# Performance work log

Hardware: AMD Instinct MI355X
Metric: run time of the kernel (lower is better)

The kernel has to match this reference:

```python
import jax, jax.numpy as jnp
import numpy as np

B, T, D, H, C = 128, 1024, 256, 256, 128


def setup_inputs() -> dict:
    key = jax.random.key(0)
    ks = jax.random.split(key, 10)
    s = 0.02  # scale down randn init so sigmoid/tanh don't saturate numerically
    inp = {
        "x": jax.random.normal(ks[0], (B, T, D), dtype=jnp.float32),
        "W_xi": jax.random.normal(ks[1], (D, H), dtype=jnp.float32) * s,
        "W_hi": jax.random.normal(ks[2], (H, H), dtype=jnp.float32) * s,
        "b_i": jnp.zeros((H,), jnp.float32),
        "W_xf": jax.random.normal(ks[3], (D, H), dtype=jnp.float32) * s,
        "W_hf": jax.random.normal(ks[4], (H, H), dtype=jnp.float32) * s,
        "b_f": jnp.zeros((H,), jnp.float32),
        "W_xg": jax.random.normal(ks[5], (D, H), dtype=jnp.float32) * s,
        "W_hg": jax.random.normal(ks[6], (H, H), dtype=jnp.float32) * s,
        "b_g": jnp.zeros((H,), jnp.float32),
        "W_xo": jax.random.normal(ks[7], (D, H), dtype=jnp.float32) * s,
        "W_ho": jax.random.normal(ks[8], (H, H), dtype=jnp.float32) * s,
        "b_o": jnp.zeros((H,), jnp.float32),
        "W_hy": jax.random.normal(ks[9], (H, C), dtype=jnp.float32) * s,
        "b_y": jnp.zeros((C,), jnp.float32),
    }
    return inp


def reference(x, W_xi, W_hi, b_i, W_xf, W_hf, b_f, W_xg, W_hg, b_g,
              W_xo, W_ho, b_o, W_hy, b_y):
    batch, _, _ = x.shape
    hid = W_hi.shape[0]
    # Precompute all input projections for all timesteps (4 big GEMMs).
    xi = jnp.einsum("btd,dh->bth", x, W_xi) + b_i
    xf = jnp.einsum("btd,dh->bth", x, W_xf) + b_f
    xg = jnp.einsum("btd,dh->bth", x, W_xg) + b_g
    xo = jnp.einsum("btd,dh->bth", x, W_xo) + b_o
    # Time-major stacked gate pre-activations: [T, B, 4H]
    gates_x = jnp.concatenate([xi, xf, xg, xo], axis=-1).transpose(1, 0, 2)
    W_h = jnp.concatenate([W_hi, W_hf, W_hg, W_ho], axis=1)  # [H, 4H]

    def step(carry, gx_t):
        h, c = carry
        z = gx_t + h @ W_h  # [B, 4H]
        i_t = jax.nn.sigmoid(z[:, 0 * hid:1 * hid])
        f_t = jax.nn.sigmoid(z[:, 1 * hid:2 * hid])
        g_t = jnp.tanh(z[:, 2 * hid:3 * hid])
        o_t = jax.nn.sigmoid(z[:, 3 * hid:4 * hid])
        c_new = f_t * c + i_t * g_t
        h_new = o_t * jnp.tanh(c_new)
        return (h_new, c_new), None

    h0 = jnp.zeros((batch, hid), x.dtype)
    c0 = jnp.zeros((batch, hid), x.dtype)
    (h_T, _), _ = jax.lax.scan(step, (h0, c0), gates_x)
    return h_T @ W_hy + b_y
```

## Files before the change

kernel.cpp:

```cpp
#include <hip/hip_runtime.h>

using u16 = unsigned short;
using u32 = unsigned int;

typedef _Float16 f16x2 __attribute__((ext_vector_type(2)));
typedef _Float16 f16x8 __attribute__((ext_vector_type(8)));
typedef float    f32x4 __attribute__((ext_vector_type(4)));

__device__ __forceinline__ u16 f16bits(float x) {
  union { _Float16 h; u16 u; } r; r.h = (_Float16)x; return r.u;
}
__device__ __forceinline__ float h2f(u16 v) {
  union { u16 u; _Float16 h; } r; r.u = v; return (float)r.h;
}
__device__ __forceinline__ u32 pack2(float a, float b) {
  union { f16x2 h; u32 u; } r; r.h.x = (_Float16)a; r.h.y = (_Float16)b; return r.u;
}
__device__ __forceinline__ float fdot2a(u32 a, u32 b, float c) {
  union { u32 u; f16x2 h; } ua, ub; ua.u = a; ub.u = b;
#if __has_builtin(__builtin_amdgcn_fdot2)
  return __builtin_amdgcn_fdot2(ua.h, ub.h, c, false);
#else
  return c + (float)ua.h.x * (float)ub.h.x + (float)ua.h.y * (float)ub.h.y;
#endif
}
__device__ __forceinline__ float sigmoidf_(float x) { return 1.0f / (1.0f + __expf(-x)); }
__device__ __forceinline__ float tanhf_(float x)    { return 1.0f - 2.0f / (__expf(2.0f * x) + 1.0f); }

__device__ __forceinline__ f16x8 lds16(const u16* p) {
  union { uint4 u; f16x8 h; } r; r.u = *(const uint4*)p; return r.h;
}

__global__ void lstm_prep(const float* __restrict__ Wxi, const float* __restrict__ Wxf,
                          const float* __restrict__ Wxg, const float* __restrict__ Wxo,
                          const float* __restrict__ Whi, const float* __restrict__ Whf,
                          const float* __restrict__ Whg, const float* __restrict__ Who,
                          u16* __restrict__ WxT, u32* __restrict__ Whpp,
                          u32* __restrict__ h16s, float* __restrict__ c_s) {
  int idx = blockIdx.x * 256 + threadIdx.x;
  if (idx < 262144) {
    int n = idx >> 8, k = idx & 255;
    int g = n >> 8;
    const float* W = (g == 0) ? Wxi : (g == 1) ? Wxf : (g == 2) ? Wxg : Wxo;
    WxT[idx] = f16bits(W[k * 256 + (n & 255)]);
  } else if (idx < 262144 + 131072) {
    int i2 = idx - 262144;
    int e = i2 & 3, tmp = i2 >> 2;
    int t = tmp & 1023, i4 = tmp >> 10;
    int cc = i4 >> 3, pp = i4 & 7;
    int w = t >> 6, l = t & 63, q = l >> 4;
    int j = w * 64 + (l & 15) * 4 + cc;
    int kk = q * 32 + pp * 4 + e;
    int g = j >> 8, col = j & 255;
    const float* W = (g == 0) ? Whi : (g == 1) ? Whf : (g == 2) ? Whg : Who;
    u32 lo = f16bits(W[(2 * kk) * 256 + col]);
    u32 hi = f16bits(W[(2 * kk + 1) * 256 + col]);
    Whpp[i2] = lo | (hi << 16);
  } else if (idx < 262144 + 131072 + 16384) {
    h16s[idx - 393216] = 0u;
  } else if (idx < 262144 + 131072 + 16384 + 32768) {
    c_s[idx - 409600] = 0.0f;
  }
}

__global__ __launch_bounds__(256) void proj_gemm(
    const float* __restrict__ x, const u16* __restrict__ WxT,
    u16* __restrict__ gates, const float* __restrict__ bi,
    const float* __restrict__ bf, const float* __restrict__ bg,
    const float* __restrict__ bo, int t0, int tcShift) {
  __shared__ u16 Al[128 * 72];
  __shared__ u16 Bl[128 * 72];
  const int tid = threadIdx.x;
  const int lane = tid & 63, wv = tid >> 6;
  const int wr = wv >> 1, wc = wv & 1;
  const int m0 = blockIdx.x * 128, n0 = blockIdx.y * 128;
  const int tcMask = (1 << tcShift) - 1;
  f32x4 acc[4][4] = {};
  for (int k0 = 0; k0 < 256; k0 += 64) {
#pragma unroll
    for (int p = 0; p < 8; ++p) {
      int flat = p * 256 + tid;
      int r = flat >> 4, cc = flat & 15;
      int m = m0 + r;
      int b = m >> tcShift, tc = m & tcMask;
      const float4 xv = *(const float4*)(x + (size_t)(b * 1024 + t0 + tc) * 256 + k0 + cc * 4);
      uint2 w2 = make_uint2(pack2(xv.x, xv.y), pack2(xv.z, xv.w));
      *(uint2*)&Al[r * 72 + cc * 4] = w2;
    }
#pragma unroll
    for (int p = 0; p < 8; ++p) {
      int flat = p * 256 + tid;
      int r = flat >> 4, cc = flat & 15;
      uint2 w2 = *(const uint2*)(WxT + (size_t)(n0 + r) * 256 + k0 + cc * 4);
      *(uint2*)&Bl[r * 72 + cc * 4] = w2;
    }
    __syncthreads();
#pragma unroll
    for (int kk = 0; kk < 64; kk += 32) {
      f16x8 af[4], bfr[4];
#pragma unroll
      for (int i = 0; i < 4; ++i) {
        af[i]  = lds16(&Al[(wr * 64 + i * 16 + (lane & 15)) * 72 + kk + (lane >> 4) * 8]);
        bfr[i] = lds16(&Bl[(wc * 64 + i * 16 + (lane & 15)) * 72 + kk + (lane >> 4) * 8]);
      }
#pragma unroll
      for (int mi = 0; mi < 4; ++mi)
#pragma unroll
        for (int ni = 0; ni < 4; ++ni)
          acc[mi][ni] = __builtin_amdgcn_mfma_f32_16x16x32_f16(af[mi], bfr[ni], acc[mi][ni], 0, 0, 0);
    }
    __syncthreads();
  }
#pragma unroll
  for (int ni = 0; ni < 4; ++ni) {
    int n = n0 + wc * 64 + ni * 16 + (lane & 15);
    int g = n >> 8;
    const float* bp = (g == 0) ? bi : (g == 1) ? bf : (g == 2) ? bg : bo;
    float bias = bp[n & 255];
#pragma unroll
    for (int mi = 0; mi < 4; ++mi) {
#pragma unroll
      for (int ri = 0; ri < 4; ++ri) {
        int m = m0 + wr * 64 + mi * 16 + (lane >> 4) * 4 + ri;
        gates[(size_t)m * 1024 + n] = f16bits(acc[mi][ni][ri] + bias);
      }
    }
  }
}

__global__ __launch_bounds__(1024) void lstm_rec(
    const u32* __restrict__ Whpp, const u16* __restrict__ gates,
    u32* __restrict__ h16s, float* __restrict__ c_s,
    const float* __restrict__ Why, const float* __restrict__ by,
    float* __restrict__ out, int Tc, int last) {
  extern __shared__ unsigned char smem[];
  uint4* ldsW = (uint4*)smem;
  u32*   hq   = (u32*)(smem + 131072);
  float* zbuf = (float*)(smem + 131072 + 1152);
  const int b = blockIdx.x, t = threadIdx.x;
  const int l = t & 63, w = t >> 6, q = l >> 4;
  const int jb = w * 64 + (l & 15) * 4;

  u32 wreg[96];
  const uint4* Wp4 = (const uint4*)Whpp;
#pragma unroll
  for (int i4 = 0; i4 < 32; ++i4) {
    uint4 v = Wp4[i4 * 1024 + t];
    const int cc = i4 >> 3, pp = i4 & 7;
    if (pp < 6) {
      wreg[cc * 24 + pp * 4 + 0] = v.x;
      wreg[cc * 24 + pp * 4 + 1] = v.y;
      wreg[cc * 24 + pp * 4 + 2] = v.z;
      wreg[cc * 24 + pp * 4 + 3] = v.w;
    } else {
      ldsW[(cc * 2 + pp - 6) * 1024 + t] = v;
    }
  }
  if (t < 128) hq[(t >> 5) * 36 + (t & 31)] = h16s[b * 128 + t];
  float c = 0.0f;
  if (t < 256) c = c_s[b * 256 + t];
  const u16* gxp = gates + (size_t)b * Tc * 1024 + jb;
  int buf = 0;
  __syncthreads();

  for (int tc = 0; tc < Tc; ++tc) {
    uint2 gx = *(const uint2*)(gxp + (size_t)tc * 1024);
    float acc0 = 0.f, acc1 = 0.f, acc2 = 0.f, acc3 = 0.f;
    const uint4* hb = (const uint4*)(hq + buf * 144 + q * 36);
#pragma unroll
    for (int u = 0; u < 8; ++u) {
      uint4 hv = hb[u];
      uint4 w0, w1, w2, w3;
      if (u < 6) {
        w0 = make_uint4(wreg[0 * 24 + u * 4], wreg[0 * 24 + u * 4 + 1], wreg[0 * 24 + u * 4 + 2], wreg[0 * 24 + u * 4 + 3]);
        w1 = make_uint4(wreg[1 * 24 + u * 4], wreg[1 * 24 + u * 4 + 1], wreg[1 * 24 + u * 4 + 2], wreg[1 * 24 + u * 4 + 3]);
        w2 = make_uint4(wreg[2 * 24 + u * 4], wreg[2 * 24 + u * 4 + 1], wreg[2 * 24 + u * 4 + 2], wreg[2 * 24 + u * 4 + 3]);
        w3 = make_uint4(wreg[3 * 24 + u * 4], wreg[3 * 24 + u * 4 + 1], wreg[3 * 24 + u * 4 + 2], wreg[3 * 24 + u * 4 + 3]);
      } else {
        w0 = ldsW[(0 * 2 + u - 6) * 1024 + t];
        w1 = ldsW[(1 * 2 + u - 6) * 1024 + t];
        w2 = ldsW[(2 * 2 + u - 6) * 1024 + t];
        w3 = ldsW[(3 * 2 + u - 6) * 1024 + t];
      }
      acc0 = fdot2a(hv.x, w0.x, acc0); acc0 = fdot2a(hv.y, w0.y, acc0);
      acc0 = fdot2a(hv.z, w0.z, acc0); acc0 = fdot2a(hv.w, w0.w, acc0);
      acc1 = fdot2a(hv.x, w1.x, acc1); acc1 = fdot2a(hv.y, w1.y, acc1);
      acc1 = fdot2a(hv.z, w1.z, acc1); acc1 = fdot2a(hv.w, w1.w, acc1);
      acc2 = fdot2a(hv.x, w2.x, acc2); acc2 = fdot2a(hv.y, w2.y, acc2);
      acc2 = fdot2a(hv.z, w2.z, acc2); acc2 = fdot2a(hv.w, w2.w, acc2);
      acc3 = fdot2a(hv.x, w3.x, acc3); acc3 = fdot2a(hv.y, w3.y, acc3);
      acc3 = fdot2a(hv.z, w3.z, acc3); acc3 = fdot2a(hv.w, w3.w, acc3);
    }
    acc0 += __shfl_xor(acc0, 16); acc0 += __shfl_xor(acc0, 32);
    acc1 += __shfl_xor(acc1, 16); acc1 += __shfl_xor(acc1, 32);
    acc2 += __shfl_xor(acc2, 16); acc2 += __shfl_xor(acc2, 32);
    acc3 += __shfl_xor(acc3, 16); acc3 += __shfl_xor(acc3, 32);
    if (l < 16) {
      float4 z4;
      z4.x = acc0 + h2f((u16)(gx.x & 0xffff));
      z4.y = acc1 + h2f((u16)(gx.x >> 16));
      z4.z = acc2 + h2f((u16)(gx.y & 0xffff));
      z4.w = acc3 + h2f((u16)(gx.y >> 16));
      *(float4*)&zbuf[jb] = z4;
    }
    __syncthreads();
    if (t < 256) {
      float zi = zbuf[t], zf = zbuf[t + 256], zg = zbuf[t + 512], zo = zbuf[t + 768];
      float i_ = sigmoidf_(zi), f_ = sigmoidf_(zf), g_ = tanhf_(zg), o_ = sigmoidf_(zo);
      c = f_ * c + i_ * g_;
      float h_ = o_ * tanhf_(c);
      const int kk = t >> 1, qq = kk >> 5, pp = kk & 31;
      ((u16*)(hq + (buf ^ 1) * 144))[(qq * 36 + pp) * 2 + (t & 1)] = f16bits(h_);
    }
    buf ^= 1;
    __syncthreads();
  }

  if (t < 128) h16s[b * 128 + t] = hq[buf * 144 + (t >> 5) * 36 + (t & 31)];
  if (t < 256) c_s[b * 256 + t] = c;

  if (last && t < 128) {
    float acc = by[t];
    const u16* hh = (const u16*)(hq + buf * 144);
#pragma unroll 8
    for (int k = 0; k < 256; ++k) {
      float hv = h2f(hh[((k >> 6) * 36 + ((k >> 1) & 31)) * 2 + (k & 1)]);
      acc += hv * Why[k * 128 + t];
    }
    out[b * 128 + t] = acc;
  }
}

extern "C" void kernel_launch(void* const* d_in, const int* in_sizes, int n_in,
                              void* d_out, int out_size, void* d_ws, size_t ws_size,
                              hipStream_t stream) {
  const float* x   = (const float*)d_in[0];
  const float* Wxi = (const float*)d_in[1];
  const float* Whi = (const float*)d_in[2];
  const float* b_i = (const float*)d_in[3];
  const float* Wxf = (const float*)d_in[4];
  const float* Whf = (const float*)d_in[5];
  const float* b_f = (const float*)d_in[6];
  const float* Wxg = (const float*)d_in[7];
  const float* Whg = (const float*)d_in[8];
  const float* b_g = (const float*)d_in[9];
  const float* Wxo = (const float*)d_in[10];
  const float* Who = (const float*)d_in[11];
  const float* b_o = (const float*)d_in[12];
  const float* Why = (const float*)d_in[13];
  const float* b_y = (const float*)d_in[14];
  float* out = (float*)d_out;

  int Tc = 256;
  while (Tc > 32 && (size_t)128 * Tc * 1024 * 2 + 1245184ull > ws_size) Tc >>= 1;
  const int tcShift = __builtin_ctz((unsigned)Tc);
  const int nch = 1024 / Tc;

  char* wsb = (char*)d_ws;
  const size_t gbytes = (size_t)128 * Tc * 1024 * 2;
  u16*   gates16 = (u16*)wsb;
  u16*   WxT     = (u16*)(wsb + gbytes);
  u32*   Whpp    = (u32*)(wsb + gbytes + 524288);
  u32*   h16s    = (u32*)(wsb + gbytes + 1048576);
  float* c_s     = (float*)(wsb + gbytes + 1048576 + 65536);

  const int recLds = 131072 + 1152 + 4096;
  (void)hipFuncSetAttribute((const void*)lstm_rec,
                            hipFuncAttributeMaxDynamicSharedMemorySize, recLds);

  lstm_prep<<<1728, 256, 0, stream>>>(Wxi, Wxf, Wxg, Wxo, Whi, Whf, Whg, Who,
                                      WxT, Whpp, h16s, c_s);
  for (int ci = 0; ci < nch; ++ci) {
    int t0 = ci * Tc;
    proj_gemm<<<dim3(Tc, 8), 256, 0, stream>>>(x, WxT, gates16, b_i, b_f, b_g, b_o,
                                               t0, tcShift);
    lstm_rec<<<128, 1024, recLds, stream>>>(Whpp, gates16, h16s, c_s, Why, b_y, out,
                                            Tc, (ci == nch - 1) ? 1 : 0);
  }
}
```

Before: 2.254 ms.

## Assign one hidden unit's four gates per lane to drop mid-step barrier

The recurrent weight packing is remapped so each 16-lane column group computes the i/f/g/o pre-activations for a single hidden unit instead of four adjacent gate columns. Each thread can then apply the nonlinearities and cell update in registers right after the shuffle reduction, which removes the zbuf round-trip through LDS and one __syncthreads per timestep. It also keeps 7 of 8 weight chunks in registers (112 VGPRs) instead of 6, halving LDS weight traffic, and prefetches the next step's gate inputs one iteration ahead. The costs are higher register pressure and redundant activation math in all four q-lanes, with only the l<16 lanes writing h.

```diff
diff --git a/kernel.cpp b/kernel.cpp
--- a/kernel.cpp
+++ b/kernel.cpp
@@ -47,11 +47,10 @@
     int i2 = idx - 262144;
     int e = i2 & 3, tmp = i2 >> 2;
     int t = tmp & 1023, i4 = tmp >> 10;
-    int cc = i4 >> 3, pp = i4 & 7;
+    int g = i4 >> 3, pp = i4 & 7;
     int w = t >> 6, l = t & 63, q = l >> 4;
-    int j = w * 64 + (l & 15) * 4 + cc;
+    int col = w * 16 + (l & 15);
     int kk = q * 32 + pp * 4 + e;
-    int g = j >> 8, col = j & 255;
     const float* W = (g == 0) ? Whi : (g == 1) ? Whf : (g == 2) ? Whg : Who;
     u32 lo = f16bits(W[(2 * kk) * 256 + col]);
     u32 hi = f16bits(W[(2 * kk + 1) * 256 + col]);
@@ -135,52 +134,55 @@
     float* __restrict__ out, int Tc, int last) {
   extern __shared__ unsigned char smem[];
   uint4* ldsW = (uint4*)smem;
-  u32*   hq   = (u32*)(smem + 131072);
-  float* zbuf = (float*)(smem + 131072 + 1152);
+  u32*   hq   = (u32*)(smem + 65536);
   const int b = blockIdx.x, t = threadIdx.x;
   const int l = t & 63, w = t >> 6, q = l >> 4;
-  const int jb = w * 64 + (l & 15) * 4;
-
-  u32 wreg[96];
+  const int hcol = w * 16 + (l & 15);
+
+  u32 wreg[112];
   const uint4* Wp4 = (const uint4*)Whpp;
 #pragma unroll
   for (int i4 = 0; i4 < 32; ++i4) {
     uint4 v = Wp4[i4 * 1024 + t];
-    const int cc = i4 >> 3, pp = i4 & 7;
-    if (pp < 6) {
-      wreg[cc * 24 + pp * 4 + 0] = v.x;
-      wreg[cc * 24 + pp * 4 + 1] = v.y;
-      wreg[cc * 24 + pp * 4 + 2] = v.z;
-      wreg[cc * 24 + pp * 4 + 3] = v.w;
+    const int g = i4 >> 3, pp = i4 & 7;
+    if (pp < 7) {
+      wreg[g * 28 + pp * 4 + 0] = v.x;
+      wreg[g * 28 + pp * 4 + 1] = v.y;
+      wreg[g * 28 + pp * 4 + 2] = v.z;
+      wreg[g * 28 + pp * 4 + 3] = v.w;
     } else {
-      ldsW[(cc * 2 + pp - 6) * 1024 + t] = v;
-    }
-  }
-  if (t < 128) hq[(t >> 5) * 36 + (t & 31)] = h16s[b * 128 + t];
-  float c = 0.0f;
-  if (t < 256) c = c_s[b * 256 + t];
-  const u16* gxp = gates + (size_t)b * Tc * 1024 + jb;
+      ldsW[g * 1024 + t] = v;
+    }
+  }
+  if (t < 128) hq[(t >> 5) * 40 + (t & 31)] = h16s[b * 128 + t];
+  float c = c_s[b * 256 + hcol];
+  const u16* gxp = gates + (size_t)b * Tc * 1024 + hcol;
+  u16 pre0 = gxp[0], pre1 = gxp[256], pre2 = gxp[512], pre3 = gxp[768];
   int buf = 0;
   __syncthreads();
 
   for (int tc = 0; tc < Tc; ++tc) {
-    uint2 gx = *(const uint2*)(gxp + (size_t)tc * 1024);
+    const u16 cur0 = pre0, cur1 = pre1, cur2 = pre2, cur3 = pre3;
+    if (tc + 1 < Tc) {
+      const u16* gn = gxp + (size_t)(tc + 1) * 1024;
+      pre0 = gn[0]; pre1 = gn[256]; pre2 = gn[512]; pre3 = gn[768];
+    }
     float acc0 = 0.f, acc1 = 0.f, acc2 = 0.f, acc3 = 0.f;
-    const uint4* hb = (const uint4*)(hq + buf * 144 + q * 36);
+    const uint4* hb = (const uint4*)(hq + buf * 160 + q * 40);
 #pragma unroll
     for (int u = 0; u < 8; ++u) {
       uint4 hv = hb[u];
       uint4 w0, w1, w2, w3;
-      if (u < 6) {
-        w0 = make_uint4(wreg[0 * 24 + u * 4], wreg[0 * 24 + u * 4 + 1], wreg[0 * 24 + u * 4 + 2], wreg[0 * 24 + u * 4 + 3]);
-        w1 = make_uint4(wreg[1 * 24 + u * 4], wreg[1 * 24 + u * 4 + 1], wreg[1 * 24 + u * 4 + 2], wreg[1 * 24 + u * 4 + 3]);
-        w2 = make_uint4(wreg[2 * 24 + u * 4], wreg[2 * 24 + u * 4 + 1], wreg[2 * 24 + u * 4 + 2], wreg[2 * 24 + u * 4 + 3]);
-        w3 = make_uint4(wreg[3 * 24 + u * 4], wreg[3 * 24 + u * 4 + 1], wreg[3 * 24 + u * 4 + 2], wreg[3 * 24 + u * 4 + 3]);
+      if (u < 7) {
+        w0 = make_uint4(wreg[0 * 28 + u * 4], wreg[0 * 28 + u * 4 + 1], wreg[0 * 28 + u * 4 + 2], wreg[0 * 28 + u * 4 + 3]);
+        w1 = make_uint4(wreg[1 * 28 + u * 4], wreg[1 * 28 + u * 4 + 1], wreg[1 * 28 + u * 4 + 2], wreg[1 * 28 + u * 4 + 3]);
+        w2 = make_uint4(wreg[2 * 28 + u * 4], wreg[2 * 28 + u * 4 + 1], wreg[2 * 28 + u * 4 + 2], wreg[2 * 28 + u * 4 + 3]);
+        w3 = make_uint4(wreg[3 * 28 + u * 4], wreg[3 * 28 + u * 4 + 1], wreg[3 * 28 + u * 4 + 2], wreg[3 * 28 + u * 4 + 3]);
       } else {
-        w0 = ldsW[(0 * 2 + u - 6) * 1024 + t];
-        w1 = ldsW[(1 * 2 + u - 6) * 1024 + t];
-        w2 = ldsW[(2 * 2 + u - 6) * 1024 + t];
-        w3 = ldsW[(3 * 2 + u - 6) * 1024 + t];
+        w0 = ldsW[0 * 1024 + t];
+        w1 = ldsW[1 * 1024 + t];
+        w2 = ldsW[2 * 1024 + t];
+        w3 = ldsW[3 * 1024 + t];
       }
       acc0 = fdot2a(hv.x, w0.x, acc0); acc0 = fdot2a(hv.y, w0.y, acc0);
       acc0 = fdot2a(hv.z, w0.z, acc0); acc0 = fdot2a(hv.w, w0.w, acc0);
@@ -195,36 +197,30 @@
     acc1 += __shfl_xor(acc1, 16); acc1 += __shfl_xor(acc1, 32);
     acc2 += __shfl_xor(acc2, 16); acc2 += __shfl_xor(acc2, 32);
     acc3 += __shfl_xor(acc3, 16); acc3 += __shfl_xor(acc3, 32);
+    float zi = acc0 + h2f(cur0);
+    float zf = acc1 + h2f(cur1);
+    float zg = acc2 + h2f(cur2);
+    float zo = acc3 + h2f(cur3);
+    float i_ = sigmoidf_(zi), f_ = sigmoidf_(zf), g_ = tanhf_(zg), o_ = sigmoidf_(zo);
+    c = f_ * c + i_ * g_;
+    float h_ = o_ * tanhf_(c);
     if (l < 16) {
-      float4 z4;
-      z4.x = acc0 + h2f((u16)(gx.x & 0xffff));
-      z4.y = acc1 + h2f((u16)(gx.x >> 16));
-      z4.z = acc2 + h2f((u16)(gx.y & 0xffff));
-      z4.w = acc3 + h2f((u16)(gx.y >> 16));
-      *(float4*)&zbuf[jb] = z4;
-    }
-    __syncthreads();
-    if (t < 256) {
-      float zi = zbuf[t], zf = zbuf[t + 256], zg = zbuf[t + 512], zo = zbuf[t + 768];
-      float i_ = sigmoidf_(zi), f_ = sigmoidf_(zf), g_ = tanhf_(zg), o_ = sigmoidf_(zo);
-      c = f_ * c + i_ * g_;
-      float h_ = o_ * tanhf_(c);
-      const int kk = t >> 1, qq = kk >> 5, pp = kk & 31;
-      ((u16*)(hq + (buf ^ 1) * 144))[(qq * 36 + pp) * 2 + (t & 1)] = f16bits(h_);
+      const int kk = hcol >> 1;
+      ((u16*)hq)[((buf ^ 1) * 160 + (kk >> 5) * 40 + (kk & 31)) * 2 + (hcol & 1)] = f16bits(h_);
     }
     buf ^= 1;
     __syncthreads();
   }
 
-  if (t < 128) h16s[b * 128 + t] = hq[buf * 144 + (t >> 5) * 36 + (t & 31)];
-  if (t < 256) c_s[b * 256 + t] = c;
+  if (t < 128) h16s[b * 128 + t] = hq[buf * 160 + (t >> 5) * 40 + (t & 31)];
+  if (l < 16) c_s[b * 256 + hcol] = c;
 
   if (last && t < 128) {
     float acc = by[t];
-    const u16* hh = (const u16*)(hq + buf * 144);
+    const u16* hh = (const u16*)(hq + buf * 160);
 #pragma unroll 8
     for (int k = 0; k < 256; ++k) {
-      float hv = h2f(hh[((k >> 6) * 36 + ((k >> 1) & 31)) * 2 + (k & 1)]);
+      float hv = h2f(hh[((k >> 6) * 40 + ((k >> 1) & 31)) * 2 + (k & 1)]);
       acc += hv * Why[k * 128 + t];
     }
     out[b * 128 + t] = acc;
@@ -264,7 +260,7 @@
   u32*   h16s    = (u32*)(wsb + gbytes + 1048576);
   float* c_s     = (float*)(wsb + gbytes + 1048576 + 65536);
 
-  const int recLds = 131072 + 1152 + 4096;
+  const int recLds = 65536 + 1280;
   (void)hipFuncSetAttribute((const void*)lstm_rec,
                             hipFuncAttributeMaxDynamicSharedMemorySize, recLds);
 
```

Result: slower. 4.365 ms (+93.7%).

## Repartition LSTM recurrence so each wave owns a K-quarter and reduces via LDS

Applied to the files above, without the earlier changes.

Changes the recurrent matvec partition so each 4-wave group covers 256 gate columns. Each wave handles one quarter of the hidden dimension, and h values are broadcast with readlane instead of per-lane LDS vector reads. Cross-lane shuffle reductions are replaced by per-wave partial sums written to LDS and summed by the 256 cell threads. Gate pre-activations are now written interleaved (i,f,g,o per column) and prefetched one step ahead. The change also adds s_setprio around the dot-product loop. In exchange it uses more LDS and adds a four-way LDS reduction in the serial section.

```diff
diff --git a/kernel.cpp b/kernel.cpp
--- a/kernel.cpp
+++ b/kernel.cpp
@@ -48,9 +48,10 @@
     int e = i2 & 3, tmp = i2 >> 2;
     int t = tmp & 1023, i4 = tmp >> 10;
     int cc = i4 >> 3, pp = i4 & 7;
-    int w = t >> 6, l = t & 63, q = l >> 4;
-    int j = w * 64 + (l & 15) * 4 + cc;
-    int kk = q * 32 + pp * 4 + e;
+    int w = t >> 6, l = t & 63;
+    int grp = w >> 2, qw = w & 3;
+    int j = grp * 256 + l * 4 + cc;
+    int kk = qw * 32 + pp * 4 + e;
     int g = j >> 8, col = j & 255;
     const float* W = (g == 0) ? Whi : (g == 1) ? Whf : (g == 2) ? Whg : Who;
     u32 lo = f16bits(W[(2 * kk) * 256 + col]);
@@ -117,12 +118,13 @@
     int g = n >> 8;
     const float* bp = (g == 0) ? bi : (g == 1) ? bf : (g == 2) ? bg : bo;
     float bias = bp[n & 255];
+    const int nperm = (n & 255) * 4 + g;
 #pragma unroll
     for (int mi = 0; mi < 4; ++mi) {
 #pragma unroll
       for (int ri = 0; ri < 4; ++ri) {
         int m = m0 + wr * 64 + mi * 16 + (lane >> 4) * 4 + ri;
-        gates[(size_t)m * 1024 + n] = f16bits(acc[mi][ni][ri] + bias);
+        gates[(size_t)m * 1024 + nperm] = f16bits(acc[mi][ni][ri] + bias);
       }
     }
   }
@@ -134,12 +136,13 @@
     const float* __restrict__ Why, const float* __restrict__ by,
     float* __restrict__ out, int Tc, int last) {
   extern __shared__ unsigned char smem[];
-  uint4* ldsW = (uint4*)smem;
-  u32*   hq   = (u32*)(smem + 131072);
-  float* zbuf = (float*)(smem + 131072 + 1152);
+  uint4* ldsW  = (uint4*)smem;
+  u32*   hq    = (u32*)(smem + 131072);
+  float* zpart = (float*)(smem + 131072 + 1280);
   const int b = blockIdx.x, t = threadIdx.x;
-  const int l = t & 63, w = t >> 6, q = l >> 4;
-  const int jb = w * 64 + (l & 15) * 4;
+  const int l = t & 63, w = t >> 6;
+  const int grp = w >> 2, qw = w & 3;
+  const int jb = grp * 256 + l * 4;
 
   u32 wreg[96];
   const uint4* Wp4 = (const uint4*)Whpp;
@@ -153,78 +156,90 @@
       wreg[cc * 24 + pp * 4 + 2] = v.z;
       wreg[cc * 24 + pp * 4 + 3] = v.w;
     } else {
-      ldsW[(cc * 2 + pp - 6) * 1024 + t] = v;
-    }
-  }
-  if (t < 128) hq[(t >> 5) * 36 + (t & 31)] = h16s[b * 128 + t];
+      ldsW[(cc * 2 + (pp - 6)) * 1024 + t] = v;
+    }
+  }
+  if (t < 128) hq[(t >> 5) * 40 + (t & 31)] = h16s[b * 128 + t];
   float c = 0.0f;
-  if (t < 256) c = c_s[b * 256 + t];
-  const u16* gxp = gates + (size_t)b * Tc * 1024 + jb;
+  uint2 pre = make_uint2(0u, 0u);
+  const u16* gxp = gates + (size_t)b * Tc * 1024 + t * 4;
+  if (t < 256) {
+    c = c_s[b * 256 + t];
+    pre = *(const uint2*)gxp;
+  }
   int buf = 0;
   __syncthreads();
 
   for (int tc = 0; tc < Tc; ++tc) {
-    uint2 gx = *(const uint2*)(gxp + (size_t)tc * 1024);
-    float acc0 = 0.f, acc1 = 0.f, acc2 = 0.f, acc3 = 0.f;
-    const uint4* hb = (const uint4*)(hq + buf * 144 + q * 36);
-#pragma unroll
-    for (int u = 0; u < 8; ++u) {
-      uint4 hv = hb[u];
-      uint4 w0, w1, w2, w3;
-      if (u < 6) {
-        w0 = make_uint4(wreg[0 * 24 + u * 4], wreg[0 * 24 + u * 4 + 1], wreg[0 * 24 + u * 4 + 2], wreg[0 * 24 + u * 4 + 3]);
-        w1 = make_uint4(wreg[1 * 24 + u * 4], wreg[1 * 24 + u * 4 + 1], wreg[1 * 24 + u * 4 + 2], wreg[1 * 24 + u * 4 + 3]);
-        w2 = make_uint4(wreg[2 * 24 + u * 4], wreg[2 * 24 + u * 4 + 1], wreg[2 * 24 + u * 4 + 2], wreg[2 * 24 + u * 4 + 3]);
-        w3 = make_uint4(wreg[3 * 24 + u * 4], wreg[3 * 24 + u * 4 + 1], wreg[3 * 24 + u * 4 + 2], wreg[3 * 24 + u * 4 + 3]);
-      } else {
-        w0 = ldsW[(0 * 2 + u - 6) * 1024 + t];
-        w1 = ldsW[(1 * 2 + u - 6) * 1024 + t];
-        w2 = ldsW[(2 * 2 + u - 6) * 1024 + t];
-        w3 = ldsW[(3 * 2 + u - 6) * 1024 + t];
-      }
-      acc0 = fdot2a(hv.x, w0.x, acc0); acc0 = fdot2a(hv.y, w0.y, acc0);
-      acc0 = fdot2a(hv.z, w0.z, acc0); acc0 = fdot2a(hv.w, w0.w, acc0);
-      acc1 = fdot2a(hv.x, w1.x, acc1); acc1 = fdot2a(hv.y, w1.y, acc1);
-      acc1 = fdot2a(hv.z, w1.z, acc1); acc1 = fdot2a(hv.w, w1.w, acc1);
-      acc2 = fdot2a(hv.x, w2.x, acc2); acc2 = fdot2a(hv.y, w2.y, acc2);
-      acc2 = fdot2a(hv.z, w2.z, acc2); acc2 = fdot2a(hv.w, w2.w, acc2);
-      acc3 = fdot2a(hv.x, w3.x, acc3); acc3 = fdot2a(hv.y, w3.y, acc3);
-      acc3 = fdot2a(hv.z, w3.z, acc3); acc3 = fdot2a(hv.w, w3.w, acc3);
-    }
-    acc0 += __shfl_xor(acc0, 16); acc0 += __shfl_xor(acc0, 32);
-    acc1 += __shfl_xor(acc1, 16); acc1 += __shfl_xor(acc1, 32);
-    acc2 += __shfl_xor(acc2, 16); acc2 += __shfl_xor(acc2, 32);
-    acc3 += __shfl_xor(acc3, 16); acc3 += __shfl_xor(acc3, 32);
-    if (l < 16) {
-      float4 z4;
-      z4.x = acc0 + h2f((u16)(gx.x & 0xffff));
-      z4.y = acc1 + h2f((u16)(gx.x >> 16));
-      z4.z = acc2 + h2f((u16)(gx.y & 0xffff));
-      z4.w = acc3 + h2f((u16)(gx.y >> 16));
-      *(float4*)&zbuf[jb] = z4;
-    }
+    const uint4 hv4 = *(const uint4*)(hq + buf * 160 + qw * 40 + (l & 7) * 4);
+    u32 sh[32];
+#pragma unroll
+    for (int i = 0; i < 8; ++i) {
+      sh[4 * i + 0] = (u32)__builtin_amdgcn_readlane((int)hv4.x, i);
+      sh[4 * i + 1] = (u32)__builtin_amdgcn_readlane((int)hv4.y, i);
+      sh[4 * i + 2] = (u32)__builtin_amdgcn_readlane((int)hv4.z, i);
+      sh[4 * i + 3] = (u32)__builtin_amdgcn_readlane((int)hv4.w, i);
+    }
+    float acc[4] = {0.f, 0.f, 0.f, 0.f};
+    __builtin_amdgcn_s_setprio(1);
+#pragma unroll
+    for (int pp = 0; pp < 6; ++pp) {
+#pragma unroll
+      for (int cc = 0; cc < 4; ++cc) {
+        acc[cc] = fdot2a(sh[pp * 4 + 0], wreg[cc * 24 + pp * 4 + 0], acc[cc]);
+        acc[cc] = fdot2a(sh[pp * 4 + 1], wreg[cc * 24 + pp * 4 + 1], acc[cc]);
+        acc[cc] = fdot2a(sh[pp * 4 + 2], wreg[cc * 24 + pp * 4 + 2], acc[cc]);
+        acc[cc] = fdot2a(sh[pp * 4 + 3], wreg[cc * 24 + pp * 4 + 3], acc[cc]);
+      }
+    }
+#pragma unroll
+    for (int pp = 6; pp < 8; ++pp) {
+#pragma unroll
+      for (int cc = 0; cc < 4; ++cc) {
+        uint4 wv = ldsW[(cc * 2 + (pp - 6)) * 1024 + t];
+        acc[cc] = fdot2a(sh[pp * 4 + 0], wv.x, acc[cc]);
+        acc[cc] = fdot2a(sh[pp * 4 + 1], wv.y, acc[cc]);
+        acc[cc] = fdot2a(sh[pp * 4 + 2], wv.z, acc[cc]);
+        acc[cc] = fdot2a(sh[pp * 4 + 3], wv.w, acc[cc]);
+      }
+    }
+    __builtin_amdgcn_s_setprio(0);
+    *(float4*)&zpart[qw * 1024 + jb] = *(float4*)acc;
     __syncthreads();
     if (t < 256) {
-      float zi = zbuf[t], zf = zbuf[t + 256], zg = zbuf[t + 512], zo = zbuf[t + 768];
+      const uint2 gx = pre;
+      if (tc + 1 < Tc) pre = *(const uint2*)(gxp + (size_t)(tc + 1) * 1024);
+      float z0 = zpart[0 * 1024 + 0 * 256 + t] + zpart[1 * 1024 + 0 * 256 + t]
+               + zpart[2 * 1024 + 0 * 256 + t] + zpart[3 * 1024 + 0 * 256 + t];
+      float z1 = zpart[0 * 1024 + 1 * 256 + t] + zpart[1 * 1024 + 1 * 256 + t]
+               + zpart[2 * 1024 + 1 * 256 + t] + zpart[3 * 1024 + 1 * 256 + t];
+      float z2 = zpart[0 * 1024 + 2 * 256 + t] + zpart[1 * 1024 + 2 * 256 + t]
+               + zpart[2 * 1024 + 2 * 256 + t] + zpart[3 * 1024 + 2 * 256 + t];
+      float z3 = zpart[0 * 1024 + 3 * 256 + t] + zpart[1 * 1024 + 3 * 256 + t]
+               + zpart[2 * 1024 + 3 * 256 + t] + zpart[3 * 1024 + 3 * 256 + t];
+      float zi = z0 + h2f((u16)(gx.x & 0xffff));
+      float zf = z1 + h2f((u16)(gx.x >> 16));
+      float zg = z2 + h2f((u16)(gx.y & 0xffff));
+      float zo = z3 + h2f((u16)(gx.y >> 16));
       float i_ = sigmoidf_(zi), f_ = sigmoidf_(zf), g_ = tanhf_(zg), o_ = sigmoidf_(zo);
       c = f_ * c + i_ * g_;
       float h_ = o_ * tanhf_(c);
-      const int kk = t >> 1, qq = kk >> 5, pp = kk & 31;
-      ((u16*)(hq + (buf ^ 1) * 144))[(qq * 36 + pp) * 2 + (t & 1)] = f16bits(h_);
+      const int kk = t >> 1;
+      ((u16*)(hq + (buf ^ 1) * 160))[((kk >> 5) * 40 + (kk & 31)) * 2 + (t & 1)] = f16bits(h_);
     }
     buf ^= 1;
     __syncthreads();
   }
 
-  if (t < 128) h16s[b * 128 + t] = hq[buf * 144 + (t >> 5) * 36 + (t & 31)];
+  if (t < 128) h16s[b * 128 + t] = hq[buf * 160 + (t >> 5) * 40 + (t & 31)];
   if (t < 256) c_s[b * 256 + t] = c;
 
   if (last && t < 128) {
     float acc = by[t];
-    const u16* hh = (const u16*)(hq + buf * 144);
+    const u16* hh = (const u16*)(hq + buf * 160);
 #pragma unroll 8
     for (int k = 0; k < 256; ++k) {
-      float hv = h2f(hh[((k >> 6) * 36 + ((k >> 1) & 31)) * 2 + (k & 1)]);
+      float hv = h2f(hh[((k >> 6) * 40 + ((k >> 1) & 31)) * 2 + (k & 1)]);
       acc += hv * Why[k * 128 + t];
     }
     out[b * 128 + t] = acc;
@@ -264,7 +279,7 @@
   u32*   h16s    = (u32*)(wsb + gbytes + 1048576);
   float* c_s     = (float*)(wsb + gbytes + 1048576 + 65536);
 
-  const int recLds = 131072 + 1152 + 4096;
+  const int recLds = 131072 + 1280 + 16384;
   (void)hipFuncSetAttribute((const void*)lstm_rec,
                             hipFuncAttributeMaxDynamicSharedMemorySize, recLds);
 
```

Result: faster. 2.194 ms (-2.7%).
